# Optimization experiments

Measured on AMD Instinct MI355X. Metric: run time of the kernel, lower is better.

Reference implementation:

```python
import jax, jax.numpy as jnp
import numpy as np

EMBEDDING_DIM = 10
FEATURE_DIMS = [4, 4, 4, 4, 4, 4, 4, 4, 4, 4, 4, 4, 2, 2, 1, 4, 1, 1, 1, 1, 1, 1, 2]
F = len(FEATURE_DIMS)          # 23 features
DMAX = max(FEATURE_DIMS)       # 4, pad width
TOTAL = sum(FEATURE_DIMS)      # 63 input columns
B = 524288


def _packed_meta():
    dims = np.array(FEATURE_DIMS)
    offsets = np.concatenate([[0], np.cumsum(dims)[:-1]])
    # gather index [F, DMAX]: column j of feature i maps to offsets[i]+min(j, dim-1)
    j = np.arange(DMAX)[None, :]
    idx = offsets[:, None] + np.minimum(j, dims[:, None] - 1)
    # validity mask [F, DMAX]: zero out padded weight columns
    mask = (j < dims[:, None]).astype(np.float32)
    return idx.astype(np.int32), mask


def setup_inputs() -> dict:
    key = jax.random.key(0)
    k_x, k_w, k_b = jax.random.split(key, 3)
    idx_np, mask_np = _packed_meta()
    x = jax.random.normal(k_x, (B, TOTAL), dtype=jnp.float32)
    # packed block-diagonal weights [F, DMAX, E]; padded rows zeroed so they
    # contribute nothing (faithful to 23 separate nn.Linear layers)
    W = jax.random.normal(k_w, (F, DMAX, EMBEDDING_DIM), dtype=jnp.float32) * 0.3
    W = W * jnp.asarray(mask_np)[:, :, None]
    b = jax.random.normal(k_b, (F, EMBEDDING_DIM), dtype=jnp.float32) * 0.1
    idx = jnp.asarray(idx_np)
    return {"input": x, "W": W, "b": b, "idx": idx}


def reference(input, W, b, idx):
    # gather each feature's slice, padded to DMAX: [B, F, DMAX]
    x_pad = input[:, idx]
    # grouped small GEMM across all 23 features in one einsum: [B, F, E]
    out = jnp.einsum('bfd,fde->bfe', x_pad, W) + b[None, :, :]
    return out
```

## Files before the change

kernel.cpp:

```cpp
#include <hip/hip_runtime.h>


#define PROJ_B     524288
#define PROJ_TOTAL 65
#define PROJ_F     23
#define PROJ_DMAX  4
#define PROJ_E     10
#define PROJ_COLS  (PROJ_F * PROJ_E)
#define PROJ_HALF  (PROJ_COLS / 2)
#define ROWS       64
#define TILE_DW    (ROWS * PROJ_TOTAL)
#define TILE_F4    (TILE_DW / 4)

__global__ __launch_bounds__(256, 8)
void Projection_5171140624940_kernel(const float* __restrict__ x,
                                     const float* __restrict__ W,
                                     const float* __restrict__ bias,
                                     const int*   __restrict__ idx,
                                     float*       __restrict__ out) {
    __shared__ float xs[TILE_DW];

    const int tid = threadIdx.x;
    const long long b0 = (long long)blockIdx.x * ROWS;

    const float4* __restrict__ src = (const float4*)(x + b0 * PROJ_TOTAL);
    float4* dst = (float4*)xs;
    #pragma unroll
    for (int i = 0; i < 4; ++i)
        dst[i * 256 + tid] = src[i * 256 + tid];
    if (tid < TILE_F4 - 4 * 256)
        dst[4 * 256 + tid] = src[4 * 256 + tid];

    const int c2 = tid & 127;
    const int ro = tid >> 7;
    const bool active = (c2 < PROJ_HALF);
    const int c  = active ? (c2 * 2) : 0;
    const int f  = c / PROJ_E;
    const int e  = c - f * PROJ_E;

    const int4 id = *(const int4*)(idx + f * PROJ_DMAX);
    const float* __restrict__ Wf = W + f * (PROJ_DMAX * PROJ_E) + e;
    const float2 w0 = *(const float2*)(Wf + 0 * PROJ_E);
    const float2 w1 = *(const float2*)(Wf + 1 * PROJ_E);
    const float2 w2 = *(const float2*)(Wf + 2 * PROJ_E);
    const float2 w3 = *(const float2*)(Wf + 3 * PROJ_E);
    const float2 bb = *(const float2*)(bias + f * PROJ_E + e);

    __syncthreads();

    if (active) {
        float* op = out + (b0 + ro) * PROJ_COLS + c;
        #pragma unroll 4
        for (int r = ro; r < ROWS; r += 2) {
            const float* __restrict__ xr = xs + r * PROJ_TOTAL;
            const float x0 = xr[id.x];
            const float x1 = xr[id.y];
            const float x2 = xr[id.z];
            const float x3 = xr[id.w];
            float2 acc = bb;
            acc.x = fmaf(x0, w0.x, fmaf(x1, w1.x, fmaf(x2, w2.x, fmaf(x3, w3.x, acc.x))));
            acc.y = fmaf(x0, w0.y, fmaf(x1, w1.y, fmaf(x2, w2.y, fmaf(x3, w3.y, acc.y))));
            *(float2*)op = acc;
            op += 2 * PROJ_COLS;
        }
    }
}

extern "C" void kernel_launch(void* const* d_in, const int* in_sizes, int n_in,
                              void* d_out, int out_size, void* d_ws, size_t ws_size,
                              hipStream_t stream) {
    const float* x    = (const float*)d_in[0];
    const float* W    = (const float*)d_in[1];
    const float* bias = (const float*)d_in[2];
    const int*   idx  = (const int*)d_in[3];
    float* out = (float*)d_out;

    const int grid  = PROJ_B / ROWS;
    const int block = 256;

    Projection_5171140624940_kernel<<<grid, block, 0, stream>>>(x, W, bias, idx, out);
}
```

Baseline: 569.3 us.

## Write output as float4 nontemporal stores over row pairs

Each thread now owns one float4 slot spanning a pair of output rows (460 floats per pair = 115 float4), so stores become 16-byte nontemporal writes instead of 8-byte writes. Each lane may straddle two features or two rows, so it gathers two sets of four x values and selects per element. Per-thread weight and bias registers grow to 16 and 4 values, and the occupancy hint in launch bounds drops from 8 to 4. The aim is to cut store instruction count and cache pollution on the write-bound output, at the cost of more register pressure and extra LDS reads.

```diff
diff --git a/kernel.cpp b/kernel.cpp
--- a/kernel.cpp
+++ b/kernel.cpp
@@ -7,12 +7,16 @@
 #define PROJ_DMAX  4
 #define PROJ_E     10
 #define PROJ_COLS  (PROJ_F * PROJ_E)
-#define PROJ_HALF  (PROJ_COLS / 2)
+#define PAIR_DW    (2 * PROJ_COLS)
+#define PAIR_F4    (PAIR_DW / 4)
 #define ROWS       64
+#define NPAIR      (ROWS / 2)
 #define TILE_DW    (ROWS * PROJ_TOTAL)
 #define TILE_F4    (TILE_DW / 4)
 
-__global__ __launch_bounds__(256, 8)
+typedef float f32x4 __attribute__((ext_vector_type(4)));
+
+__global__ __launch_bounds__(256, 4)
 void Projection_5171140624940_kernel(const float* __restrict__ x,
                                      const float* __restrict__ W,
                                      const float* __restrict__ bias,
@@ -23,45 +27,69 @@
     const int tid = threadIdx.x;
     const long long b0 = (long long)blockIdx.x * ROWS;
 
-    const float4* __restrict__ src = (const float4*)(x + b0 * PROJ_TOTAL);
-    float4* dst = (float4*)xs;
+    const f32x4* __restrict__ src = (const f32x4*)(x + b0 * PROJ_TOTAL);
+    f32x4* dst = (f32x4*)xs;
     #pragma unroll
     for (int i = 0; i < 4; ++i)
         dst[i * 256 + tid] = src[i * 256 + tid];
     if (tid < TILE_F4 - 4 * 256)
         dst[4 * 256 + tid] = src[4 * 256 + tid];
 
-    const int c2 = tid & 127;
-    const int ro = tid >> 7;
-    const bool active = (c2 < PROJ_HALF);
-    const int c  = active ? (c2 * 2) : 0;
-    const int f  = c / PROJ_E;
-    const int e  = c - f * PROJ_E;
+    const int k0 = tid & 127;
+    const int pg = tid >> 7;
+    const bool active = (k0 < PAIR_F4);
+    const int k  = active ? k0 : (PAIR_F4 - 1);
 
-    const int4 id = *(const int4*)(idx + f * PROJ_DMAX);
-    const float* __restrict__ Wf = W + f * (PROJ_DMAX * PROJ_E) + e;
-    const float2 w0 = *(const float2*)(Wf + 0 * PROJ_E);
-    const float2 w1 = *(const float2*)(Wf + 1 * PROJ_E);
-    const float2 w2 = *(const float2*)(Wf + 2 * PROJ_E);
-    const float2 w3 = *(const float2*)(Wf + 3 * PROJ_E);
-    const float2 bb = *(const float2*)(bias + f * PROJ_E + e);
+    int rj[4], fj[4], ej[4];
+    #pragma unroll
+    for (int j = 0; j < 4; ++j) {
+        const int g = 4 * k + j;
+        const int r = (g >= PROJ_COLS) ? 1 : 0;
+        const int c = g - PROJ_COLS * r;
+        const int f = c / PROJ_E;
+        rj[j] = r; fj[j] = f; ej[j] = c - f * PROJ_E;
+    }
+    const int fA = fj[0], rA = rj[0];
+    const int fB = fj[3], rB = rj[3];
+    bool useB[4];
+    #pragma unroll
+    for (int j = 0; j < 4; ++j)
+        useB[j] = (fj[j] != fA) | (rj[j] != rA);
+
+    const int4 idA = *(const int4*)(idx + fA * PROJ_DMAX);
+    const int4 idB = *(const int4*)(idx + fB * PROJ_DMAX);
+    float w[4][4], bb[4];
+    #pragma unroll
+    for (int j = 0; j < 4; ++j) {
+        const float* __restrict__ Wf = W + fj[j] * (PROJ_DMAX * PROJ_E) + ej[j];
+        #pragma unroll
+        for (int d = 0; d < 4; ++d) w[j][d] = Wf[d * PROJ_E];
+        bb[j] = bias[fj[j] * PROJ_E + ej[j]];
+    }
 
     __syncthreads();
 
     if (active) {
-        float* op = out + (b0 + ro) * PROJ_COLS + c;
-        #pragma unroll 4
-        for (int r = ro; r < ROWS; r += 2) {
-            const float* __restrict__ xr = xs + r * PROJ_TOTAL;
-            const float x0 = xr[id.x];
-            const float x1 = xr[id.y];
-            const float x2 = xr[id.z];
-            const float x3 = xr[id.w];
-            float2 acc = bb;
-            acc.x = fmaf(x0, w0.x, fmaf(x1, w1.x, fmaf(x2, w2.x, fmaf(x3, w3.x, acc.x))));
-            acc.y = fmaf(x0, w0.y, fmaf(x1, w1.y, fmaf(x2, w2.y, fmaf(x3, w3.y, acc.y))));
-            *(float2*)op = acc;
-            op += 2 * PROJ_COLS;
+        #pragma unroll 2
+        for (int p = pg; p < NPAIR; p += 2) {
+            const float* __restrict__ xA = xs + (2 * p + rA) * PROJ_TOTAL;
+            const float* __restrict__ xB = xs + (2 * p + rB) * PROJ_TOTAL;
+            const float xa0 = xA[idA.x], xa1 = xA[idA.y],
+                        xa2 = xA[idA.z], xa3 = xA[idA.w];
+            const float xb0 = xB[idB.x], xb1 = xB[idB.y],
+                        xb2 = xB[idB.z], xb3 = xB[idB.w];
+            f32x4 o;
+            #pragma unroll
+            for (int j = 0; j < 4; ++j) {
+                const float v0 = useB[j] ? xb0 : xa0;
+                const float v1 = useB[j] ? xb1 : xa1;
+                const float v2 = useB[j] ? xb2 : xa2;
+                const float v3 = useB[j] ? xb3 : xa3;
+                o[j] = fmaf(v0, w[j][0], fmaf(v1, w[j][1],
+                        fmaf(v2, w[j][2], fmaf(v3, w[j][3], bb[j]))));
+            }
+            f32x4* optr = (f32x4*)(out + (b0 + 2 * p) * PROJ_COLS) + k;
+            __builtin_nontemporal_store(o, optr);
         }
     }
 }
```

New measurement: 596.9 us. +4.9%, slower.
